# Kernel optimization log

Hardware: AMD Instinct MI355X
Metric: run time of the kernel (lower is better)

Reference implementation:

```python
import jax, jax.numpy as jnp
import numpy as np

D_MODEL = 1024

def setup_inputs() -> dict:
    key = jax.random.key(0)
    ks = jax.random.split(key, 7)
    B, T, D = 4, 4096, D_MODEL
    s = 1.0 / np.sqrt(D)
    return {
        "x": jax.random.normal(ks[0], (B, T, D), dtype=jnp.float32),
        "Wq": jax.random.normal(ks[1], (D, D), dtype=jnp.float32) * s,
        "bq": jax.random.normal(ks[2], (D,), dtype=jnp.float32) * 0.01,
        "Wk": jax.random.normal(ks[3], (D, D), dtype=jnp.float32) * s,
        "bk": jax.random.normal(ks[4], (D,), dtype=jnp.float32) * 0.01,
        "Wv": jax.random.normal(ks[5], (D, D), dtype=jnp.float32) * s,
        "bv": jax.random.normal(ks[6], (D,), dtype=jnp.float32) * 0.01,
    }

def reference(x, Wq, bq, Wk, bk, Wv, bv):
    # x: [B, T, D]; Linear weights stored [out, in] like torch -> x @ W.T + b
    D = x.shape[-1]
    T = x.shape[1]
    scale = jnp.sqrt(jnp.asarray(D, dtype=x.dtype))
    Q = jnp.einsum('btd,ed->bte', x, Wq) + bq
    K = jnp.einsum('btd,ed->bte', x, Wk) + bk
    V = jnp.einsum('btd,ed->bte', x, Wv) + bv
    scores = jnp.einsum('bqd,bkd->bqk', Q, K) / scale  # [B, T, T]
    causal = jnp.tril(jnp.ones((T, T), dtype=bool))    # True = keep (q >= k)
    neg_inf = jnp.asarray(-jnp.inf, dtype=scores.dtype)
    scores = jnp.where(causal, scores, neg_inf)
    probs = jax.nn.softmax(scores, axis=-1)
    return jnp.einsum('bqk,bkd->bqd', probs, V)
```

## Files before the change

### kernel.cpp

```cpp
#include <hip/hip_runtime.h>
#include <hip/hip_bf16.h>
#include <math.h>


typedef __bf16 bf16;
typedef __bf16 bf16x8 __attribute__((ext_vector_type(8)));
typedef float  f32x4  __attribute__((ext_vector_type(4)));

#define LOG2E 1.4426950408889634f

static constexpr size_t OFF_XB   = 0;
static constexpr size_t OFF_WQB  = 33554432;
static constexpr size_t OFF_WKB  = 35651584;
static constexpr size_t OFF_WVB  = 37748736;
static constexpr size_t OFF_Q    = 39845888;
static constexpr size_t OFF_K    = 73400320;
static constexpr size_t OFF_VT   = 106954752;
static constexpr size_t OFF_S    = 140509184;
static constexpr size_t OFF_PSUM = 209715200;
static constexpr size_t OFF_LINV = 211812352;

typedef __attribute__((address_space(1))) void gvoid_t;
typedef __attribute__((address_space(3))) void lvoid_t;

__device__ __forceinline__ void gload16(const void* g, void* l) {
  __builtin_amdgcn_global_load_lds((gvoid_t*)g, (lvoid_t*)l, 16, 0, 0);
}

#define PRIO1() __builtin_amdgcn_s_setprio(1)
#define PRIO0() __builtin_amdgcn_s_setprio(0)
#define BAR()   __builtin_amdgcn_s_barrier()
#define LGKM0() asm volatile("s_waitcnt lgkmcnt(0)" ::: "memory")
#define LGKM8() asm volatile("s_waitcnt lgkmcnt(8)" ::: "memory")
#define VM0()   asm volatile("s_waitcnt vmcnt(0)" ::: "memory")
#define VM4()   asm volatile("s_waitcnt vmcnt(4)" ::: "memory")

struct Ctx { int tid, lane, quad, col16, wr, wc, wcol; };
__device__ __forceinline__ Ctx mk_ctx() {
  Ctx c; c.tid = (int)threadIdx.x; c.lane = c.tid & 63;
  int w = c.tid >> 6;
  c.quad = c.lane >> 4; c.col16 = c.lane & 15;
  c.wr = (w >> 1) * 64; c.wc = (w & 1) * 64; c.wcol = w & 1;
  return c;
}

__device__ __forceinline__ void stage_tile(const bf16* g, long ld, bf16* s, int tid) {
  int lane = tid & 63, w = tid >> 6;
  const bf16* gp = g + (long)(lane >> 2) * ld + (long)(lane & 3) * 8;
  long step = 16 * ld;
  gload16(gp + (long)(2 * w) * step,     s + (2 * w) * 512);
  gload16(gp + (long)(2 * w + 1) * step, s + (2 * w + 1) * 512);
}

__device__ __forceinline__ void mfma_step(const bf16* sA, const bf16* sB,
                                          const Ctx& c, f32x4 acc[4][4]) {
  bf16x8 a[4], b[4];
#pragma unroll
  for (int i = 0; i < 4; ++i) {
    a[i] = *(const bf16x8*)(sA + ((c.wr + i * 16 + c.col16) * 32 + c.quad * 8));
    b[i] = *(const bf16x8*)(sB + ((c.wc + i * 16 + c.col16) * 32 + c.quad * 8));
  }
#pragma unroll
  for (int i = 0; i < 4; ++i)
#pragma unroll
    for (int j = 0; j < 4; ++j)
      acc[i][j] = __builtin_amdgcn_mfma_f32_16x16x32_bf16(a[i], b[j], acc[i][j], 0, 0, 0);
}

__device__ __forceinline__ void zero_acc(f32x4 acc[4][4]) {
  f32x4 z = {0.f, 0.f, 0.f, 0.f};
#pragma unroll
  for (int i = 0; i < 4; ++i)
#pragma unroll
    for (int j = 0; j < 4; ++j) acc[i][j] = z;
}

__device__ __forceinline__ int tridec(int i) {
  int qt = (int)((sqrtf(8.0f * (float)i + 1.0f) - 1.0f) * 0.5f);
  while ((qt + 1) * (qt + 2) / 2 <= i) ++qt;
  while (qt * (qt + 1) / 2 > i) --qt;
  return qt;
}

struct CC { int soff, raOff, rbOff, lofs; };
__device__ __forceinline__ CC mk_cc(int tid) {
  CC c;
  int lane = tid & 63, w = tid >> 6;
  int quad = lane >> 4, col16 = lane & 15;
  int wrow = (w >> 2) << 7, wcol = (w & 3) << 6;
  c.soff = ((tid >> 3) << 10) + (((tid & 7) ^ (((tid >> 5) & 1) << 1)) << 3);
  int cS = (quad << 3) ^ (((col16 >> 2) & 1) << 4);
  c.raOff = ((wrow + col16) << 6) + cS;
  c.rbOff = ((wcol + col16) << 6) + cS;
  c.lofs = w << 9;
  return c;
}

__device__ __forceinline__ void stg(const bf16* g, int kofs, bf16* l, const CC& c) {
  const bf16* g0 = g + kofs + c.soff;
  gload16(g0,         l + c.lofs);
  gload16(g0 + 65536, l + c.lofs + 4096);
}

__device__ __forceinline__ void read_a(const bf16* buf, const CC& c, int h, bf16x8 a[8]) {
#pragma unroll
  for (int f = 0; f < 4; ++f)
#pragma unroll
    for (int kk = 0; kk < 2; ++kk)
      a[f * 2 + kk] = *(const bf16x8*)(buf + c.raOff + h * 4096 + f * 1024 + kk * 32);
}

__device__ __forceinline__ void read_b(const bf16* buf, const CC& c, int cc, bf16x8 bb[4]) {
#pragma unroll
  for (int g = 0; g < 2; ++g)
#pragma unroll
    for (int kk = 0; kk < 2; ++kk)
      bb[g * 2 + kk] = *(const bf16x8*)(buf + c.rbOff + cc * 2048 + g * 1024 + kk * 32);
}

__device__ __forceinline__ void mfma16(const bf16x8 a[8], const bf16x8 bb[4],
                                       int h, int cc, f32x4 acc[8][4]) {
#pragma unroll
  for (int f = 0; f < 4; ++f)
#pragma unroll
    for (int g = 0; g < 2; ++g)
#pragma unroll
      for (int kk = 0; kk < 2; ++kk)
        acc[h * 4 + f][cc * 2 + g] = __builtin_amdgcn_mfma_f32_16x16x32_bf16(
            a[f * 2 + kk], bb[g * 2 + kk], acc[h * 4 + f][cc * 2 + g], 0, 0, 0);
}

__device__ __forceinline__ void zero8x4(f32x4 acc[8][4]) {
  f32x4 z = {0.f, 0.f, 0.f, 0.f};
#pragma unroll
  for (int i = 0; i < 8; ++i)
#pragma unroll
    for (int j = 0; j < 4; ++j) acc[i][j] = z;
}

template <int NT>
__device__ __forceinline__ void gemm256_core(const bf16* __restrict__ Ag,
                                             const bf16* __restrict__ Bg,
                                             bf16* sA0, bf16* sA1,
                                             bf16* sB0, bf16* sB1,
                                             const CC& c, f32x4 acc[8][4]) {
  stg(Ag, 0,           sA0, c); stg(Ag, 131072,      sA0 + 8192, c);
  stg(Bg, 0,           sB0, c); stg(Bg, 131072,      sB0 + 8192, c);
  stg(Bg, 64,          sB1, c); stg(Bg, 64 + 131072, sB1 + 8192, c);
  VM4(); BAR();

  bf16x8 a[8], b0[4], b1[4];
#pragma unroll 1
  for (int i = 0; i < NT / 2 - 1; ++i) {
    const int k1 = (2 * i + 1) << 6, k2 = k1 + 64, k3 = k1 + 128;
    read_a(sA0, c, 0, a); read_b(sB0, c, 0, b0);
    stg(Ag, k1, sA1, c);
    LGKM8(); BAR(); LGKM0();
    PRIO1(); mfma16(a, b0, 0, 0, acc); PRIO0(); BAR();
    read_b(sB0, c, 1, b1);
    stg(Ag, k1 + 131072, sA1 + 8192, c);
    BAR(); LGKM0();
    PRIO1(); mfma16(a, b1, 0, 1, acc); PRIO0(); BAR();
    read_a(sA0, c, 1, a);
    stg(Bg, k2, sB0, c);
    BAR(); LGKM0();
    PRIO1(); mfma16(a, b1, 1, 1, acc); PRIO0(); BAR();
    stg(Bg, k2 + 131072, sB0 + 8192, c);
    BAR();
    PRIO1(); mfma16(a, b0, 1, 0, acc); PRIO0();
    VM4(); BAR();
    read_a(sA1, c, 0, a); read_b(sB1, c, 0, b0);
    stg(Ag, k2, sA0, c);
    LGKM8(); BAR(); LGKM0();
    PRIO1(); mfma16(a, b0, 0, 0, acc); PRIO0(); BAR();
    read_b(sB1, c, 1, b1);
    stg(Ag, k2 + 131072, sA0 + 8192, c);
    BAR(); LGKM0();
    PRIO1(); mfma16(a, b1, 0, 1, acc); PRIO0(); BAR();
    read_a(sA1, c, 1, a);
    stg(Bg, k3, sB1, c);
    BAR(); LGKM0();
    PRIO1(); mfma16(a, b1, 1, 1, acc); PRIO0(); BAR();
    stg(Bg, k3 + 131072, sB1 + 8192, c);
    BAR();
    PRIO1(); mfma16(a, b0, 1, 0, acc); PRIO0();
    VM4(); BAR();
  }
  {
    const int k1 = (NT - 1) << 6;
    read_a(sA0, c, 0, a); read_b(sB0, c, 0, b0);
    stg(Ag, k1, sA1, c);
    LGKM8(); BAR(); LGKM0();
    PRIO1(); mfma16(a, b0, 0, 0, acc); PRIO0(); BAR();
    read_b(sB0, c, 1, b1);
    stg(Ag, k1 + 131072, sA1 + 8192, c);
    BAR(); LGKM0();
    PRIO1(); mfma16(a, b1, 0, 1, acc); PRIO0(); BAR();
    read_a(sA0, c, 1, a);
    BAR(); LGKM0();
    PRIO1(); mfma16(a, b1, 1, 1, acc); PRIO0(); BAR();
    BAR();
    PRIO1(); mfma16(a, b0, 1, 0, acc); PRIO0();
    VM0(); BAR();
    read_a(sA1, c, 0, a); read_b(sB1, c, 0, b0);
    LGKM8(); BAR(); LGKM0();
    PRIO1(); mfma16(a, b0, 0, 0, acc); PRIO0(); BAR();
    read_b(sB1, c, 1, b1);
    BAR(); LGKM0();
    PRIO1(); mfma16(a, b1, 0, 1, acc); PRIO0(); BAR();
    read_a(sA1, c, 1, a);
    BAR(); LGKM0();
    PRIO1(); mfma16(a, b1, 1, 1, acc); PRIO0();
    mfma16(a, b0, 1, 0, acc);
  }
}


__global__ __launch_bounds__(256) void cvt_all(const float* __restrict__ x,
                                               const float* __restrict__ Wq,
                                               const float* __restrict__ Wk,
                                               const float* __restrict__ Wv,
                                               bf16* __restrict__ xb,
                                               bf16* __restrict__ wqb,
                                               bf16* __restrict__ wkb,
                                               bf16* __restrict__ wvb) {
  int b = (int)blockIdx.x;
  const float* in; bf16* out; long base;
  if (b < 8192)      { in = x;  out = xb;  base = (long)b * 2048; }
  else if (b < 8704) { in = Wq; out = wqb; base = (long)(b - 8192) * 2048; }
  else if (b < 9216) { in = Wk; out = wkb; base = (long)(b - 8704) * 2048; }
  else               { in = Wv; out = wvb; base = (long)(b - 9216) * 2048; }
  long i = base + (long)threadIdx.x * 8;
  float4 f0 = *(const float4*)(in + i);
  float4 f1 = *(const float4*)(in + i + 4);
  bf16x8 h;
  h[0] = (bf16)f0.x; h[1] = (bf16)f0.y; h[2] = (bf16)f0.z; h[3] = (bf16)f0.w;
  h[4] = (bf16)f1.x; h[5] = (bf16)f1.y; h[6] = (bf16)f1.z; h[7] = (bf16)f1.w;
  *(bf16x8*)(out + i) = h;
}

__global__ __launch_bounds__(512, 2) void qkv_gemm(const bf16* __restrict__ X,
                                                   const bf16* __restrict__ Wq,
                                                   const bf16* __restrict__ Wk,
                                                   const bf16* __restrict__ Wv,
                                                   const float* __restrict__ bq,
                                                   const float* __restrict__ bk,
                                                   const float* __restrict__ bv,
                                                   bf16* __restrict__ Q,
                                                   bf16* __restrict__ K,
                                                   bf16* __restrict__ Vt) {
  __shared__ __align__(16) bf16 lds[4][16384];
  const int tid = (int)threadIdx.x;
  const CC c = mk_cc(tid);
  int b0i = (int)blockIdx.x;
  int b = (b0i & 7) * 96 + (b0i >> 3);
  const bf16 *Ag, *Bg;
  const bool is_vt = (b >= 512);
  if (!is_vt) {
    int isK = b >> 8, rem = b & 255;
    Ag = X + (long)(rem >> 2) * 262144;
    Bg = (isK ? Wk : Wq) + (long)(rem & 3) * 262144;
  } else {
    int rem = b - 512;
    Ag = Wv + (long)((rem >> 4) & 3) * 262144;
    Bg = X + (long)(rem >> 6) * 4194304 + (long)(rem & 15) * 262144;
  }
  f32x4 acc[8][4];
  zero8x4(acc);
  gemm256_core<16>(Ag, Bg, lds[0], lds[1], lds[2], lds[3], c, acc);

  const int lane = tid & 63, w = tid >> 6;
  const int quad = lane >> 4, col16 = lane & 15;
  const int wrow = (w >> 2) << 7, wcol = (w & 3) << 6;
  if (!is_vt) {
    int isK = b >> 8, rem = b & 255;
    long r0 = (long)(rem >> 2) * 256, c0 = (long)(rem & 3) * 256;
    const float* bias = isK ? bk : bq;
    bf16* out = isK ? K : Q;
#pragma unroll
    for (int n = 0; n < 4; ++n) {
      int col = (int)c0 + wcol + (n >> 1) * 32 + (n & 1) * 16 + col16;
      float bb = bias[col];
#pragma unroll
      for (int m = 0; m < 8; ++m) {
        long rowb = r0 + wrow + (m >> 2) * 64 + (m & 3) * 16 + quad * 4;
#pragma unroll
        for (int r = 0; r < 4; ++r)
          out[(rowb + r) * 1024 + col] = (bf16)(acc[m][n][r] + bb);
      }
    }
  } else {
    int rem = b - 512;
    int z = rem >> 6;
    long r0 = (long)((rem >> 4) & 3) * 256, c0 = (long)(rem & 15) * 256;
    bf16* out = Vt + (long)z * 4194304;
#pragma unroll
    for (int m = 0; m < 8; ++m) {
      long rowb = r0 + wrow + (m >> 2) * 64 + (m & 3) * 16 + quad * 4;
      float bb[4];
#pragma unroll
      for (int r = 0; r < 4; ++r) bb[r] = bv[rowb + r];
#pragma unroll
      for (int n = 0; n < 4; ++n) {
        int col = (int)c0 + wcol + (n >> 1) * 32 + (n & 1) * 16 + col16;
#pragma unroll
        for (int r = 0; r < 4; ++r)
          out[(rowb + r) * 4096 + col] = (bf16)(acc[m][n][r] + bb[r]);
      }
    }
  }
}

__global__ __launch_bounds__(256) void s_gemm(const bf16* __restrict__ Q,
                                              const bf16* __restrict__ K,
                                              bf16* __restrict__ S,
                                              float* __restrict__ psum) {
  __shared__ __align__(16) bf16 sA[2][128 * 32], sB[2][128 * 32];
  __shared__ float sred[2][128];
  Ctx c = mk_ctx();
  int ti = blockIdx.x, z = blockIdx.z;
  int qt = tridec(ti);
  int kt = ti - qt * (qt + 1) / 2;
  long q0 = (long)qt * 128, k0 = (long)kt * 128;
  const bf16* Ab = Q + (long)z * 4194304 + q0 * 1024;
  const bf16* Bb = K + (long)z * 4194304 + k0 * 1024;
  f32x4 acc[4][4]; zero_acc(acc);
  for (int k = 0; k < 1024; k += 64) {
    stage_tile(Ab + k,      1024, sA[0], c.tid);
    stage_tile(Ab + k + 32, 1024, sA[1], c.tid);
    stage_tile(Bb + k,      1024, sB[0], c.tid);
    stage_tile(Bb + k + 32, 1024, sB[1], c.tid);
    __syncthreads();
    mfma_step(sA[0], sB[0], c, acc);
    mfma_step(sA[1], sB[1], c, acc);
    __syncthreads();
  }
  bf16* st = S + ((long)z * 528 + ti) * 16384;
  const bool diag = (qt == kt);
  float rs[4][4];
#pragma unroll
  for (int i = 0; i < 4; ++i) {
#pragma unroll
    for (int r = 0; r < 4; ++r) {
      int row_l = c.wr + i * 16 + c.quad * 4 + r;
      float s = 0.f;
#pragma unroll
      for (int j = 0; j < 4; ++j) {
        int col_l = c.wc + j * 16 + c.col16;
        float p = exp2f(acc[i][j][r] * (0.03125f * LOG2E));
        if (diag && col_l > row_l) p = 0.0f;
        bf16 h = (bf16)p;
        st[row_l * 128 + col_l] = h;
        s += (float)h;
      }
      rs[i][r] = s;
    }
  }
#pragma unroll
  for (int i = 0; i < 4; ++i)
#pragma unroll
    for (int r = 0; r < 4; ++r)
#pragma unroll
      for (int m = 1; m <= 8; m <<= 1)
        rs[i][r] += __shfl_xor(rs[i][r], m);
  if (c.col16 == 0) {
#pragma unroll
    for (int i = 0; i < 4; ++i)
#pragma unroll
      for (int r = 0; r < 4; ++r)
        sred[c.wcol][c.wr + i * 16 + c.quad * 4 + r] = rs[i][r];
  }
  __syncthreads();
  if (c.tid < 128)
    psum[((long)z * 4096 + q0 + c.tid) * 32 + kt] = sred[0][c.tid] + sred[1][c.tid];
}

__global__ __launch_bounds__(256) void inv_sums(const float* __restrict__ psum,
                                                float* __restrict__ linv) {
  long i = (long)blockIdx.x * 256 + threadIdx.x;
  int q = (int)(i & 4095);
  int nt = (q >> 7) + 1;
  const float* ps = psum + i * 32;
  float l = 0.f;
  for (int t = 0; t < nt; ++t) l += ps[t];
  linv[i] = 1.0f / l;
}

__global__ __launch_bounds__(256) void o_gemm(const bf16* __restrict__ S,
                                              const bf16* __restrict__ Vt,
                                              const float* __restrict__ linv,
                                              float* __restrict__ out) {
  __shared__ __align__(16) bf16 sA[2][128 * 32], sB[2][128 * 32];
  Ctx c = mk_ctx();
  int b = (int)blockIdx.x;
  int z = b & 3, et = (b >> 2) & 7, q0i = (b >> 5) & 7, gen = b >> 8;
  int qt = (gen == 0) ? q0i : (gen == 1) ? 15 - q0i
         : (gen == 2) ? 16 + q0i : 31 - q0i;
  long q0 = (long)qt * 128, e0 = (long)et * 128;
  const bf16* Bb = Vt + (long)z * 4194304 + e0 * 4096;
  long tribase = ((long)z * 528 + (long)qt * (qt + 1) / 2) * 16384;
  f32x4 acc[4][4]; zero_acc(acc);
  int kend = (qt + 1) * 128;
  for (int k = 0; k < kend; k += 64) {
    const bf16* Ab = S + tribase + (long)(k >> 7) * 16384 + (k & 127);
    stage_tile(Ab,      128, sA[0], c.tid);
    stage_tile(Ab + 32, 128, sA[1], c.tid);
    stage_tile(Bb + k,      4096, sB[0], c.tid);
    stage_tile(Bb + k + 32, 4096, sB[1], c.tid);
    __syncthreads();
    mfma_step(sA[0], sB[0], c, acc);
    mfma_step(sA[1], sB[1], c, acc);
    __syncthreads();
  }
  long zq = (long)z * 4096 + q0;
#pragma unroll
  for (int i = 0; i < 4; ++i) {
    int rowb = c.wr + i * 16 + c.quad * 4;
    float li[4];
#pragma unroll
    for (int r = 0; r < 4; ++r) li[r] = linv[zq + rowb + r];
#pragma unroll
    for (int j = 0; j < 4; ++j) {
      int col = c.wc + j * 16 + c.col16;
#pragma unroll
      for (int r = 0; r < 4; ++r)
        out[(zq + rowb + r) * 1024 + e0 + col] = acc[i][j][r] * li[r];
    }
  }
}

extern "C" void kernel_launch(void* const* d_in, const int* in_sizes, int n_in,
                              void* d_out, int out_size, void* d_ws, size_t ws_size,
                              hipStream_t stream) {
  (void)in_sizes; (void)n_in; (void)out_size; (void)ws_size;
  const float* x  = (const float*)d_in[0];
  const float* Wq = (const float*)d_in[1];
  const float* bq = (const float*)d_in[2];
  const float* Wk = (const float*)d_in[3];
  const float* bk = (const float*)d_in[4];
  const float* Wv = (const float*)d_in[5];
  const float* bv = (const float*)d_in[6];

  char* ws = (char*)d_ws;
  bf16*  xb   = (bf16*)(ws + OFF_XB);
  bf16*  wqb  = (bf16*)(ws + OFF_WQB);
  bf16*  wkb  = (bf16*)(ws + OFF_WKB);
  bf16*  wvb  = (bf16*)(ws + OFF_WVB);
  bf16*  Qb   = (bf16*)(ws + OFF_Q);
  bf16*  Kb   = (bf16*)(ws + OFF_K);
  bf16*  Vtb  = (bf16*)(ws + OFF_VT);
  bf16*  Sb   = (bf16*)(ws + OFF_S);
  float* psum = (float*)(ws + OFF_PSUM);
  float* linv = (float*)(ws + OFF_LINV);

  cvt_all<<<9728, 256, 0, stream>>>(x, Wq, Wk, Wv, xb, wqb, wkb, wvb);
  qkv_gemm<<<768, 512, 0, stream>>>(xb, wqb, wkb, wvb, bq, bk, bv, Qb, Kb, Vtb);
  s_gemm<<<dim3(528, 1, 4), 256, 0, stream>>>(Qb, Kb, Sb, psum);
  inv_sums<<<64, 256, 0, stream>>>(psum, linv);
  o_gemm<<<1024, 256, 0, stream>>>(Sb, Vtb, linv, (float*)d_out);
}
```

Measured before the change: 486.6 us.

## Retile causal score GEMM to 256x256 blocks using shared gemm256 core

The QK^T score kernel moves from 128x128 tiles with 256 threads to 256x256 tiles with 512 threads, reusing the pipelined gemm256_core. It maps each 256 tile back onto four 128-tile outputs and skips storing the fully masked upper quadrant on diagonal tiles. The block index is swizzled across batches so neighbouring blocks spread over XCDs. The LDS read swizzle for the shared core also changes to a full 3-bit XOR pattern to cut bank conflicts. Larger tiles raise data reuse but compute some masked work on diagonals and use more registers per thread.

```diff
diff --git a/kernel.cpp b/kernel.cpp
--- a/kernel.cpp
+++ b/kernel.cpp
@@ -82,16 +82,18 @@
   return qt;
 }
 
-struct CC { int soff, raOff, rbOff, lofs; };
+struct CC { int soff, ra0, ra1, rb0, rb1, lofs; };
 __device__ __forceinline__ CC mk_cc(int tid) {
   CC c;
   int lane = tid & 63, w = tid >> 6;
   int quad = lane >> 4, col16 = lane & 15;
   int wrow = (w >> 2) << 7, wcol = (w & 3) << 6;
-  c.soff = ((tid >> 3) << 10) + (((tid & 7) ^ (((tid >> 5) & 1) << 1)) << 3);
-  int cS = (quad << 3) ^ (((col16 >> 2) & 1) << 4);
-  c.raOff = ((wrow + col16) << 6) + cS;
-  c.rbOff = ((wcol + col16) << 6) + cS;
+  int c7 = col16 & 7;
+  c.soff = ((tid >> 3) << 10) + (((tid & 7) ^ ((tid >> 3) & 7)) << 3);
+  c.ra0 = ((wrow + col16) << 6) + ((quad ^ c7) << 3);
+  c.ra1 = ((wrow + col16) << 6) + (((4 | quad) ^ c7) << 3);
+  c.rb0 = ((wcol + col16) << 6) + ((quad ^ c7) << 3);
+  c.rb1 = ((wcol + col16) << 6) + (((4 | quad) ^ c7) << 3);
   c.lofs = w << 9;
   return c;
 }
@@ -104,18 +106,18 @@
 
 __device__ __forceinline__ void read_a(const bf16* buf, const CC& c, int h, bf16x8 a[8]) {
 #pragma unroll
-  for (int f = 0; f < 4; ++f)
-#pragma unroll
-    for (int kk = 0; kk < 2; ++kk)
-      a[f * 2 + kk] = *(const bf16x8*)(buf + c.raOff + h * 4096 + f * 1024 + kk * 32);
+  for (int f = 0; f < 4; ++f) {
+    a[f * 2 + 0] = *(const bf16x8*)(buf + c.ra0 + h * 4096 + f * 1024);
+    a[f * 2 + 1] = *(const bf16x8*)(buf + c.ra1 + h * 4096 + f * 1024);
+  }
 }
 
 __device__ __forceinline__ void read_b(const bf16* buf, const CC& c, int cc, bf16x8 bb[4]) {
 #pragma unroll
-  for (int g = 0; g < 2; ++g)
-#pragma unroll
-    for (int kk = 0; kk < 2; ++kk)
-      bb[g * 2 + kk] = *(const bf16x8*)(buf + c.rbOff + cc * 2048 + g * 1024 + kk * 32);
+  for (int g = 0; g < 2; ++g) {
+    bb[g * 2 + 0] = *(const bf16x8*)(buf + c.rb0 + cc * 2048 + g * 1024);
+    bb[g * 2 + 1] = *(const bf16x8*)(buf + c.rb1 + cc * 2048 + g * 1024);
+  }
 }
 
 __device__ __forceinline__ void mfma16(const bf16x8 a[8], const bf16x8 bb[4],
@@ -311,68 +313,76 @@
   }
 }
 
-__global__ __launch_bounds__(256) void s_gemm(const bf16* __restrict__ Q,
-                                              const bf16* __restrict__ K,
-                                              bf16* __restrict__ S,
-                                              float* __restrict__ psum) {
-  __shared__ __align__(16) bf16 sA[2][128 * 32], sB[2][128 * 32];
-  __shared__ float sred[2][128];
-  Ctx c = mk_ctx();
-  int ti = blockIdx.x, z = blockIdx.z;
-  int qt = tridec(ti);
-  int kt = ti - qt * (qt + 1) / 2;
-  long q0 = (long)qt * 128, k0 = (long)kt * 128;
-  const bf16* Ab = Q + (long)z * 4194304 + q0 * 1024;
-  const bf16* Bb = K + (long)z * 4194304 + k0 * 1024;
-  f32x4 acc[4][4]; zero_acc(acc);
-  for (int k = 0; k < 1024; k += 64) {
-    stage_tile(Ab + k,      1024, sA[0], c.tid);
-    stage_tile(Ab + k + 32, 1024, sA[1], c.tid);
-    stage_tile(Bb + k,      1024, sB[0], c.tid);
-    stage_tile(Bb + k + 32, 1024, sB[1], c.tid);
-    __syncthreads();
-    mfma_step(sA[0], sB[0], c, acc);
-    mfma_step(sA[1], sB[1], c, acc);
-    __syncthreads();
-  }
-  bf16* st = S + ((long)z * 528 + ti) * 16384;
-  const bool diag = (qt == kt);
-  float rs[4][4];
-#pragma unroll
-  for (int i = 0; i < 4; ++i) {
-#pragma unroll
-    for (int r = 0; r < 4; ++r) {
-      int row_l = c.wr + i * 16 + c.quad * 4 + r;
-      float s = 0.f;
-#pragma unroll
-      for (int j = 0; j < 4; ++j) {
-        int col_l = c.wc + j * 16 + c.col16;
-        float p = exp2f(acc[i][j][r] * (0.03125f * LOG2E));
-        if (diag && col_l > row_l) p = 0.0f;
+__global__ __launch_bounds__(512, 2) void s_gemm(const bf16* __restrict__ Q,
+                                                 const bf16* __restrict__ K,
+                                                 bf16* __restrict__ S,
+                                                 float* __restrict__ psum) {
+  __shared__ __align__(16) bf16 lds[4][16384];
+  __shared__ float sred[8][128];
+  const int tid = (int)threadIdx.x;
+  const CC c = mk_cc(tid);
+  int b0i = (int)blockIdx.x;
+  int b = (b0i & 7) * 68 + (b0i >> 3);
+  int z = b & 3, ti = b >> 2;
+  int QT = tridec(ti);
+  int KT = ti - QT * (QT + 1) / 2;
+  const bf16* Ag = Q + (long)z * 4194304 + (long)QT * 262144;
+  const bf16* Bg = K + (long)z * 4194304 + (long)KT * 262144;
+  f32x4 acc[8][4];
+  zero8x4(acc);
+  gemm256_core<16>(Ag, Bg, lds[0], lds[1], lds[2], lds[3], c, acc);
+
+  const int lane = tid & 63, w = tid >> 6;
+  const int quad = lane >> 4, col16 = lane & 15;
+  const int rh = w >> 2, ch = (w & 3) >> 1;
+  const int wcol64 = (w & 1) << 6;
+  const bool diag = (QT == KT);
+  const bool skip = diag && (rh == 0) && (ch == 1);
+  const bool mask = diag && (rh == ch);
+  const int qt128 = 2 * QT + rh, kt128 = 2 * KT + ch;
+  bf16* st = S + ((long)z * 528 + (long)(qt128 * (qt128 + 1) / 2 + kt128)) * 16384;
+  float rs[8][4];
+#pragma unroll
+  for (int m = 0; m < 8; ++m)
+#pragma unroll
+    for (int r = 0; r < 4; ++r) rs[m][r] = 0.f;
+#pragma unroll
+  for (int m = 0; m < 8; ++m) {
+    int row_l = (m >> 2) * 64 + (m & 3) * 16 + quad * 4;
+#pragma unroll
+    for (int n = 0; n < 4; ++n) {
+      int col_l = wcol64 + (n >> 1) * 32 + (n & 1) * 16 + col16;
+#pragma unroll
+      for (int r = 0; r < 4; ++r) {
+        float p = exp2f(acc[m][n][r] * (0.03125f * LOG2E));
+        if (mask && col_l > row_l + r) p = 0.0f;
         bf16 h = (bf16)p;
-        st[row_l * 128 + col_l] = h;
-        s += (float)h;
+        if (!skip) st[(row_l + r) * 128 + col_l] = h;
+        rs[m][r] += (float)h;
       }
-      rs[i][r] = s;
     }
   }
 #pragma unroll
-  for (int i = 0; i < 4; ++i)
+  for (int m = 0; m < 8; ++m)
 #pragma unroll
     for (int r = 0; r < 4; ++r)
 #pragma unroll
-      for (int m = 1; m <= 8; m <<= 1)
-        rs[i][r] += __shfl_xor(rs[i][r], m);
-  if (c.col16 == 0) {
-#pragma unroll
-    for (int i = 0; i < 4; ++i)
+      for (int msk = 1; msk <= 8; msk <<= 1)
+        rs[m][r] += __shfl_xor(rs[m][r], msk);
+  if (col16 == 0) {
+#pragma unroll
+    for (int m = 0; m < 8; ++m)
 #pragma unroll
       for (int r = 0; r < 4; ++r)
-        sred[c.wcol][c.wr + i * 16 + c.quad * 4 + r] = rs[i][r];
+        sred[w][(m >> 2) * 64 + (m & 3) * 16 + quad * 4 + r] = rs[m][r];
   }
   __syncthreads();
-  if (c.tid < 128)
-    psum[((long)z * 4096 + q0 + c.tid) * 32 + kt] = sred[0][c.tid] + sred[1][c.tid];
+  {
+    int rh2 = (tid >> 7) & 1, row_l = tid & 127, ch2 = tid >> 8;
+    int base = rh2 * 4 + ch2 * 2;
+    psum[((long)z * 4096 + (long)QT * 256 + rh2 * 128 + row_l) * 32 + 2 * KT + ch2] =
+        sred[base][row_l] + sred[base + 1][row_l];
+  }
 }
 
 __global__ __launch_bounds__(256) void inv_sums(const float* __restrict__ psum,
@@ -455,7 +465,7 @@
 
   cvt_all<<<9728, 256, 0, stream>>>(x, Wq, Wk, Wv, xb, wqb, wkb, wvb);
   qkv_gemm<<<768, 512, 0, stream>>>(xb, wqb, wkb, wvb, bq, bk, bv, Qb, Kb, Vtb);
-  s_gemm<<<dim3(528, 1, 4), 256, 0, stream>>>(Qb, Kb, Sb, psum);
+  s_gemm<<<544, 512, 0, stream>>>(Qb, Kb, Sb, psum);
   inv_sums<<<64, 256, 0, stream>>>(psum, linv);
   o_gemm<<<1024, 256, 0, stream>>>(Sb, Vtb, linv, (float*)d_out);
 }
```

New measurement: 485.6 us. Within noise of the previous version (-0.2%).
